# Performance work log

Measured on AMD Instinct MI355X. Metric: run time of the kernel, lower is better.

## Reference

```python
import jax, jax.numpy as jnp
import numpy as np

B, S, E, H = 2, 2048, 1024, 16
D = E // H  # head_dim = 64


def setup_inputs() -> dict:
    key = jax.random.key(0)
    ks = jax.random.split(key, 4)
    return {
        "hidden_states": jax.random.normal(ks[0], (B, S, E), jnp.float32),
        "qk_weight": jax.random.normal(ks[1], (E, 2 * E), jnp.float32) * 0.02,
        "qk_bias": jnp.zeros((2 * E,), jnp.float32),
        "v_weight": jax.random.normal(ks[2], (E, E), jnp.float32) * 0.02,
        "v_resid_gain": jnp.ones((), jnp.float32),
        "v_skip_gain": jnp.ones((), jnp.float32),
        "proj_weight": jax.random.normal(ks[3], (E, E), jnp.float32) * 0.02,
        "proj_resid_gain": jnp.ones((), jnp.float32),
        "proj_skip_gain": jnp.ones((), jnp.float32),
        "attn_mat_resid_gain": jnp.ones((H,), jnp.float32),
        "attn_mat_skip_gain": jnp.ones((H,), jnp.float32),
        "centre_attn_gain": jnp.ones((H,), jnp.float32),
    }


def reference(hidden_states, qk_weight, qk_bias, v_weight, v_resid_gain,
              v_skip_gain, proj_weight, proj_resid_gain, proj_skip_gain,
              attn_mat_resid_gain, attn_mat_skip_gain, centre_attn_gain):
    b, s, e = hidden_states.shape
    dt = hidden_states.dtype
    eye_e = jnp.eye(e, dtype=dt)

    # qk_attn: MyConv1D (standard linear), split into query/key
    qk = hidden_states @ qk_weight + qk_bias
    q, k = jnp.split(qk, 2, axis=-1)
    # v_attn: skip MyConv1D -> x @ (resid_gain * W + skip_gain * I), no bias
    v = hidden_states @ (v_resid_gain * v_weight + v_skip_gain * eye_e)

    def split_heads(t):  # [b,s,e] -> [b,h,s,d]
        return t.reshape(b, s, H, D).transpose(0, 2, 1, 3)

    q, k, v = split_heads(q), split_heads(k), split_heads(v)

    # scaled causal attention scores
    scores = jnp.einsum('bhqd,bhkd->bhqk', q, k) / jnp.asarray(D, dt) ** 0.5
    causal = jnp.tril(jnp.ones((s, s), bool))
    scores = jnp.where(causal, scores, jnp.finfo(dt).min)
    attn = jax.nn.softmax(scores, axis=-1)

    # shaped attention: gain-mix softmax probs with identity and causal-uniform
    uniform = jnp.tril(jnp.ones((s, s), dt) / jnp.arange(1, s + 1, dtype=dt)[:, None])
    g_r = attn_mat_resid_gain[None, :, None, None]
    g_s = attn_mat_skip_gain[None, :, None, None]
    g_c = centre_attn_gain[None, :, None, None]
    new_attn = g_r * attn + g_s * jnp.eye(s, dtype=dt) - g_c * uniform

    ctx = jnp.einsum('bhqk,bhkd->bhqd', new_attn, v)
    ctx = ctx.transpose(0, 2, 1, 3).reshape(b, s, e)  # merge heads
    # c_proj: skip MyConv1D, no bias
    out = ctx @ (proj_resid_gain * proj_weight + proj_skip_gain * eye_e)
    return out
```

## Files before the change

kernel.cpp:

```cpp
#include <hip/hip_runtime.h>

typedef __bf16 bf16;
typedef __attribute__((ext_vector_type(8))) __bf16 bf16x8;
typedef __attribute__((ext_vector_type(4))) float f32x4;

union U16x8 { uint4 u; bf16 h[8]; };
union Pack4 { uint2 u2; bf16 h[4]; };

#define QSCALE 0.18033688011112042f

__device__ __forceinline__ void async16(const bf16* g, bf16* l) {
    __builtin_amdgcn_global_load_lds((const __attribute__((address_space(1))) void*)g,
                                     (__attribute__((address_space(3))) void*)l, 16, 0, 0);
}

__device__ const int QT_OF[40] = {15,15,15,15,14,14,14,14,13,13,13,13,12,12,12,12,
                                  11,11,11,10,10,10,9,9,9,8,8,8,7,7,6,6,5,5,4,4,3,2,1,0};
__device__ const int CK_OF[40] = {0,1,2,3,0,1,2,3,0,1,2,3,0,1,2,3,
                                  0,1,2,0,1,2,0,1,2,0,1,2,0,1,0,1,0,1,0,1,0,0,0,0};
__device__ const int BASE_OF[16] = {39,38,37,36,34,32,30,28,25,22,19,16,12,8,4,0};

__global__ void prep(const float* __restrict__ hs, bf16* __restrict__ hsb,
                     const float* __restrict__ qkw, const float* __restrict__ vw,
                     const float* __restrict__ pw, bf16* __restrict__ qkvT,
                     bf16* __restrict__ pwT, float* __restrict__ csum,
                     const float* __restrict__ vrg, const float* __restrict__ vsg,
                     const float* __restrict__ prg, const float* __restrict__ psg) {
    const int K = 1024;
    int bx = blockIdx.x;
    if (bx < 8) {
        float4* p = (float4*)csum + (bx * 256 + threadIdx.x) * 16;
        #pragma unroll
        for (int i = 0; i < 16; i++) p[i] = make_float4(0.f, 0.f, 0.f, 0.f);
        return;
    }
    if (bx < 4104) {
        int i = ((bx - 8) * 256 + threadIdx.x) * 4;
        float4 f = *(const float4*)(hs + i);
        hsb[i + 0] = (bf16)f.x; hsb[i + 1] = (bf16)f.y;
        hsb[i + 2] = (bf16)f.z; hsb[i + 3] = (bf16)f.w;
        return;
    }
    int r = bx - 4104;
    int z = r < 2048 ? 0 : (r < 3072 ? 1 : 2);
    int q = z == 0 ? r : (z == 1 ? r - 2048 : r - 3072);
    int ntiles = z == 0 ? 64 : 32;
    int N = z == 0 ? 2048 : 1024;
    const float* W = z == 0 ? qkw : (z == 1 ? vw : pw);
    bf16* WT = z == 0 ? qkvT : (z == 1 ? qkvT + (size_t)2 * 1024 * 1024 : pwT);
    float g0 = z == 0 ? 1.f : (z == 1 ? vrg[0] : prg[0]);
    float g1 = z == 0 ? 0.f : (z == 1 ? vsg[0] : psg[0]);

    __shared__ float tile[32][33];
    int n0 = (q % ntiles) * 32, k0 = (q / ntiles) * 32;
    int tx = threadIdx.x & 31, ty = threadIdx.x >> 5;
    #pragma unroll
    for (int rr = 0; rr < 32; rr += 8)
        tile[ty + rr][tx] = W[(size_t)(k0 + ty + rr) * N + n0 + tx];
    __syncthreads();
    #pragma unroll
    for (int rr = 0; rr < 32; rr += 8) {
        int n = n0 + ty + rr, k = k0 + tx;
        float v = g0 * tile[tx][ty + rr] + ((n == k) ? g1 : 0.f);
        if (z == 0 && n < 1024) v *= QSCALE;
        WT[(size_t)n * K + k] = (bf16)v;
    }
}

template<int BN>
__global__ __launch_bounds__(256, 3)
void gemm_bt(const bf16* __restrict__ A, const bf16* __restrict__ BT,
             int M, int N, int K, void* __restrict__ Cout,
             bf16* __restrict__ C2T, float* __restrict__ csum,
             int mode, const float* __restrict__ aux) {
    __shared__ __align__(16) bf16 As[128][64];
    __shared__ __align__(16) bf16 Bs[BN][64];
    constexpr int JF = BN / 32;
    int bid = blockIdx.x;
    int g32 = bid & 31;
    int m0 = ((g32 & 7) * 4 + (g32 >> 3)) * 128;
    int n0 = (bid >> 5) * BN;
    int t = threadIdx.x, lane = t & 63, w = t >> 6;
    int wm = (w >> 1) * 64, wn = (w & 1) * (BN / 2);
    int lrow = lane & 15, lkg = lane >> 4;

    f32x4 acc[4][JF] = {};

    int gsw = ((lane & 7) ^ ((lane >> 3) & 7)) * 8;
    const bf16* Ab = A + (size_t)(m0 + w * 8 + (lane >> 3)) * K + gsw;
    const bf16* Bb = BT + (size_t)(n0 + w * 8 + (lane >> 3)) * K + gsw;

    for (int k0 = 0; k0 < K; k0 += 64) {
        #pragma unroll
        for (int p = 0; p < 4; p++)
            async16(Ab + (size_t)(p * 32) * K + k0, &As[p * 32 + w * 8][0]);
        #pragma unroll
        for (int p = 0; p < BN / 32; p++)
            async16(Bb + (size_t)(p * 32) * K + k0, &Bs[p * 32 + w * 8][0]);
        __syncthreads();
        #pragma unroll
        for (int ks = 0; ks < 2; ks++) {
            bf16x8 af[4], bfr[JF];
            int phys = (((4 * ks + lkg) ^ (lrow & 7)) << 3);
            #pragma unroll
            for (int i = 0; i < 4; i++) af[i] = *(const bf16x8*)&As[wm + i * 16 + lrow][phys];
            #pragma unroll
            for (int j = 0; j < JF; j++) bfr[j] = *(const bf16x8*)&Bs[wn + j * 16 + lrow][phys];
            #pragma unroll
            for (int i = 0; i < 4; i++)
                #pragma unroll
                for (int j = 0; j < JF; j++)
                    acc[i][j] = __builtin_amdgcn_mfma_f32_16x16x32_bf16(af[i], bfr[j], acc[i][j], 0, 0, 0);
        }
        __syncthreads();
    }

    int rgrp = (lane >> 4) * 4;
    #pragma unroll
    for (int i = 0; i < 4; i++) {
        #pragma unroll
        for (int j = 0; j < JF; j++) {
            int col = n0 + wn + j * 16 + lrow;
            int row0 = m0 + wm + i * 16 + rgrp;
            if (mode == 0) {
                if (col < 2048) {
                    float bb = aux[col];
                    if (col < 1024) bb *= QSCALE;
                    #pragma unroll
                    for (int reg = 0; reg < 4; reg++)
                        ((bf16*)Cout)[(size_t)(row0 + reg) * 2048 + col] = (bf16)(acc[i][j][reg] + bb);
                } else {
                    int c = col - 2048;
                    Pack4 p4;
                    #pragma unroll
                    for (int reg = 0; reg < 4; reg++) p4.h[reg] = (bf16)acc[i][j][reg];
                    *(uint2*)&C2T[(size_t)c * 4096 + row0] = p4.u2;
                }
            } else {
                #pragma unroll
                for (int reg = 0; reg < 4; reg++)
                    ((float*)Cout)[(size_t)(row0 + reg) * N + col] = acc[i][j][reg];
            }
        }
    }

    if (mode == 0 && n0 >= 2048) {
        int chunkb = (m0 + wm) >> 5;
        #pragma unroll
        for (int j = 0; j < JF; j++) {
            float s0 = 0.f, s1 = 0.f;
            #pragma unroll
            for (int reg = 0; reg < 4; reg++) {
                s0 += acc[0][j][reg] + acc[1][j][reg];
                s1 += acc[2][j][reg] + acc[3][j][reg];
            }
            s0 += __shfl_xor(s0, 16, 64); s0 += __shfl_xor(s0, 32, 64);
            s1 += __shfl_xor(s1, 16, 64); s1 += __shfl_xor(s1, 32, 64);
            if (lkg == 0) {
                int col = n0 - 2048 + wn + j * 16 + lrow;
                atomicAdd(&csum[(size_t)col * 128 + chunkb], s0);
                atomicAdd(&csum[(size_t)col * 128 + chunkb + 1], s1);
            }
        }
    }
}

__global__ __launch_bounds__(256, 3)
void flash_split(const bf16* __restrict__ qk, const bf16* __restrict__ vT,
                 bf16* __restrict__ Opart, float* __restrict__ lbuf,
                 int S, int E, int H) {
    __shared__ __align__(16) bf16 Ks[2][64][64];
    __shared__ __align__(16) bf16 Vt[2][64][64];
    __shared__ __align__(16) bf16 Ps[4][32][72];

    int item = blockIdx.x, bh = blockIdx.y;
    int qt = QT_OF[item], ck = CK_OF[item];
    int b = bh >> 4, h = bh & 15;
    int q0 = qt * 128;
    int ktstart = ck * 8;
    int nloc = min(8, 2 * (qt + 1) - ktstart);
    int t = threadIdx.x, lane = t & 63, w = t >> 6;
    int lrow = lane & 15, lkg = lane >> 4;
    const int ld = 2 * E;

    const bf16* Qg  = qk + (size_t)(b * S + q0) * ld + h * 64;
    const bf16* Kg0 = qk + (size_t)(b * S) * ld + E + h * 64;
    const bf16* Vg0 = vT + (size_t)(h * 64) * 4096 + b * 2048;

    bf16x8 qf[2][2];
    #pragma unroll
    for (int qg = 0; qg < 2; qg++)
        #pragma unroll
        for (int ks = 0; ks < 2; ks++)
            qf[qg][ks] = *(const bf16x8*)&Qg[(size_t)(32 * w + 16 * qg + lrow) * ld + ks * 32 + lkg * 8];

    f32x4 oacc[4][2] = {};
    float lrun[2] = {0.f, 0.f};

    auto stage = [&](int buf, int kt) {
        int k0 = kt * 64;
        int g = (lane & 7) ^ ((lane >> 3) & 7);
        #pragma unroll
        for (int p = 0; p < 2; p++) {
            int row = w * 8 + p * 32 + (lane >> 3);
            async16(Kg0 + (size_t)(k0 + row) * ld + g * 8, &Ks[buf][row][(lane & 7) * 8]);
            async16(Vg0 + (size_t)row * 4096 + k0 + g * 8, &Vt[buf][row][(lane & 7) * 8]);
        }
    };

    stage(0, ktstart);
    for (int kl = 0; kl < nloc; kl++) {
        int buf = kl & 1;
        int k0 = (ktstart + kl) * 64;
        __syncthreads();
        if (kl + 1 < nloc) stage(1 - buf, ktstart + kl + 1);

        bool skip0 = (k0 > q0 + 32 * w + 15);
        bool skip1 = (k0 > q0 + 32 * w + 31);
        if (skip0 && skip1) continue;

        f32x4 sacc[2][4] = {};
        #pragma unroll
        for (int ks = 0; ks < 2; ks++) {
            bf16x8 ak[4];
            int phys = (((4 * ks + lkg) ^ (lrow & 7)) << 3);
            #pragma unroll
            for (int kf = 0; kf < 4; kf++)
                ak[kf] = *(const bf16x8*)&Ks[buf][16 * kf + lrow][phys];
            #pragma unroll
            for (int kf = 0; kf < 4; kf++)
                sacc[0][kf] = __builtin_amdgcn_mfma_f32_16x16x32_bf16(ak[kf], qf[0][ks], sacc[0][kf], 0, 0, 0);
            if (!skip1)
                #pragma unroll
                for (int kf = 0; kf < 4; kf++)
                    sacc[1][kf] = __builtin_amdgcn_mfma_f32_16x16x32_bf16(ak[kf], qf[1][ks], sacc[1][kf], 0, 0, 0);
        }

        #pragma unroll
        for (int qg = 0; qg < 2; qg++) {
            if ((qg == 0 && skip0) || (qg == 1 && skip1)) continue;
            int kmin = q0 + 32 * w + 16 * qg;
            float rsum = 0.f;
            if (k0 + 63 <= kmin) {
                #pragma unroll
                for (int kf = 0; kf < 4; kf++) {
                    Pack4 p4;
                    #pragma unroll
                    for (int r = 0; r < 4; r++) {
                        float p = exp2f(sacc[qg][kf][r]);
                        rsum += p;
                        p4.h[r] = (bf16)p;
                    }
                    *(uint2*)&Ps[w][16 * qg + lrow][16 * kf + 4 * lkg] = p4.u2;
                }
            } else {
                int qrow = kmin + lrow;
                #pragma unroll
                for (int kf = 0; kf < 4; kf++) {
                    Pack4 p4;
                    #pragma unroll
                    for (int r = 0; r < 4; r++) {
                        float sv = sacc[qg][kf][r];
                        if (k0 + 16 * kf + 4 * lkg + r > qrow) sv = -1e30f;
                        float p = exp2f(sv);
                        rsum += p;
                        p4.h[r] = (bf16)p;
                    }
                    *(uint2*)&Ps[w][16 * qg + lrow][16 * kf + 4 * lkg] = p4.u2;
                }
            }
            lrun[qg] += rsum;
        }

        #pragma unroll
        for (int ks = 0; ks < 2; ks++) {
            bf16x8 av[4];
            int phys = (((4 * ks + lkg) ^ (lrow & 7)) << 3);
            #pragma unroll
            for (int df = 0; df < 4; df++)
                av[df] = *(const bf16x8*)&Vt[buf][16 * df + lrow][phys];
            #pragma unroll
            for (int qg = 0; qg < 2; qg++) {
                if ((qg == 0 && skip0) || (qg == 1 && skip1)) continue;
                bf16x8 bp = *(const bf16x8*)&Ps[w][16 * qg + lrow][ks * 32 + lkg * 8];
                #pragma unroll
                for (int df = 0; df < 4; df++)
                    oacc[df][qg] = __builtin_amdgcn_mfma_f32_16x16x32_bf16(av[df], bp, oacc[df][qg], 0, 0, 0);
            }
        }
    }

    size_t ibase = (size_t)(bh * 40 + item) * 128;
    #pragma unroll
    for (int qg = 0; qg < 2; qg++) {
        #pragma unroll
        for (int df = 0; df < 4; df++) {
            Pack4 p4;
            #pragma unroll
            for (int r = 0; r < 4; r++) p4.h[r] = (bf16)oacc[df][qg][r];
            *(uint2*)&Ps[w][16 * qg + lrow][16 * df + 4 * lkg] = p4.u2;
        }
        float l = lrun[qg];
        l += __shfl_xor(l, 16, 64);
        l += __shfl_xor(l, 32, 64);
        if (lkg == 0) lbuf[ibase + w * 32 + qg * 16 + lrow] = l;
    }
    int r_l = lane >> 1, half = lane & 1;
    bf16* orow = Opart + (ibase + w * 32 + r_l) * 64 + 32 * half;
    #pragma unroll
    for (int c = 0; c < 4; c++)
        *(uint4*)&orow[8 * c] = *(const uint4*)&Ps[w][r_l][32 * half + 8 * c];
}

__global__ void merge_combine(const bf16* __restrict__ Opart, const float* __restrict__ lbuf,
                              const bf16* __restrict__ vT, const float* __restrict__ csum,
                              const float* __restrict__ gr, const float* __restrict__ gs,
                              const float* __restrict__ gc, bf16* __restrict__ ctx) {
    const int S = 2048, E = 1024;
    int qt = blockIdx.x, bh = blockIdx.y;
    int b = bh >> 4, h = bh & 15;
    int nc = (qt >> 2) + 1, base = BASE_OF[qt];
    int q0 = qt * 128;
    int t = threadIdx.x;

    __shared__ bf16 osm[128][66];

    {
        int r = t >> 1, dh = (t & 1) * 32;
        float L = 0.f;
        for (int c = 0; c < nc; c++)
            L += lbuf[(size_t)(bh * 40 + base + c) * 128 + r];
        float inv = 1.f / L;
        float o[32] = {};
        for (int c = 0; c < nc; c++) {
            const bf16* src = Opart + ((size_t)(bh * 40 + base + c) * 128 + r) * 64 + dh;
            #pragma unroll
            for (int g = 0; g < 4; g++) {
                U16x8 u; u.u = *(const uint4*)&src[g * 8];
                #pragma unroll
                for (int j = 0; j < 8; j++) o[g * 8 + j] += (float)u.h[j];
            }
        }
        #pragma unroll
        for (int j = 0; j < 32; j++) osm[r][dh + j] = (bf16)(o[j] * inv);
    }
    __syncthreads();

    {
        int c = t & 63, sc = t >> 6;
        int col = h * 64 + c;
        int row0 = q0 + sc * 32;
        float grh = gr[h], gsh = gs[h], gch = gc[h];
        int cend = qt * 4 + sc;
        const float4* cs4 = (const float4*)(csum + (size_t)col * 128 + b * 64);
        float run = 0.f;
        #pragma unroll
        for (int g = 0; g < 16; g++) {
            float4 f = cs4[g];
            int j = g * 4;
            run += (j + 0 < cend ? f.x : 0.f) + (j + 1 < cend ? f.y : 0.f)
                 + (j + 2 < cend ? f.z : 0.f) + (j + 3 < cend ? f.w : 0.f);
        }
        const bf16* vrow = vT + (size_t)col * 4096 + b * 2048 + row0;
        U16x8 vv[4];
        #pragma unroll
        for (int g = 0; g < 4; g++) vv[g].u = *(const uint4*)&vrow[g * 8];
        bf16* cp = ctx + ((size_t)(b * S + row0)) * E + col;
        #pragma unroll
        for (int i = 0; i < 32; i++) {
            float v = (float)vv[i >> 3].h[i & 7];
            run += v;
            float pm = run / (float)(row0 + i + 1);
            cp[(size_t)i * E] = (bf16)(grh * (float)osm[sc * 32 + i][c] + gsh * v - gch * pm);
        }
    }
}

extern "C" void kernel_launch(void* const* d_in, const int* in_sizes, int n_in,
                              void* d_out, int out_size, void* d_ws, size_t ws_size,
                              hipStream_t stream) {
    const float* hs  = (const float*)d_in[0];
    const float* qkw = (const float*)d_in[1];
    const float* qkb = (const float*)d_in[2];
    const float* vw  = (const float*)d_in[3];
    const float* vrg = (const float*)d_in[4];
    const float* vsg = (const float*)d_in[5];
    const float* pw  = (const float*)d_in[6];
    const float* prg = (const float*)d_in[7];
    const float* psg = (const float*)d_in[8];
    const float* amr = (const float*)d_in[9];
    const float* ams = (const float*)d_in[10];
    const float* amc = (const float*)d_in[11];
    float* out = (float*)d_out;

    const int B = 2, S = 2048, E = 1024, H = 16, M = B * S;
    char* ws = (char*)d_ws;
    size_t off = 0;
    auto alloc = [&](size_t bytes) { void* p = ws + off; off += (bytes + 255) & ~255ull; return p; };
    bf16* hsb   = (bf16*)alloc((size_t)M * E * 2);
    bf16* qkvT  = (bf16*)alloc((size_t)3 * E * E * 2);
    bf16* pwT   = (bf16*)alloc((size_t)E * E * 2);
    bf16* qko   = (bf16*)alloc((size_t)M * 2 * E * 2);
    bf16* vT    = (bf16*)alloc((size_t)E * M * 2);
    float* csum = (float*)alloc((size_t)E * 128 * 4);
    bf16* ctxb  = (bf16*)alloc((size_t)M * E * 2);
    bf16* Opart = (bf16*)alloc((size_t)32 * 40 * 128 * 64 * 2);
    float* lbuf = (float*)alloc((size_t)32 * 40 * 128 * 4);

    prep<<<8200, 256, 0, stream>>>(hs, hsb, qkw, vw, pw, qkvT, pwT, csum, vrg, vsg, prg, psg);

    gemm_bt<128><<<32 * (3 * E / 128), 256, 0, stream>>>(
        hsb, qkvT, M, 3 * E, E, qko, vT, csum, 0, qkb);

    flash_split<<<dim3(40, 32), 256, 0, stream>>>(qko, vT, Opart, lbuf, S, E, H);
    merge_combine<<<dim3(16, 32), 256, 0, stream>>>(Opart, lbuf, vT, csum, amr, ams, amc, ctxb);

    gemm_bt<64><<<32 * (E / 64), 256, 0, stream>>>(
        ctxb, pwT, M, E, E, out, nullptr, nullptr, 2, nullptr);
}
```

Before: 206.9 us.

## Move P tile from LDS into registers via cross-lane shuffles in flash kernel

The softmax probabilities are now packed into registers and redistributed into the MFMA B-operand layout with cross-lane shuffles, instead of going through a per-wave shared-memory P buffer. The K/V buffers are merged into one 32KB array, which is reused as output staging after a barrier. Launch bounds rise from 3 to 5 blocks per SIMD. This cuts LDS footprint and LDS traffic to allow more resident blocks, but adds eight shuffles per MFMA group and may raise register pressure.

```diff
diff --git a/kernel.cpp b/kernel.cpp
--- a/kernel.cpp
+++ b/kernel.cpp
@@ -6,6 +6,8 @@
 
 union U16x8 { uint4 u; bf16 h[8]; };
 union Pack4 { uint2 u2; bf16 h[4]; };
+union PK2 { unsigned u; bf16 h[2]; };
+union BP8 { uint4 u; bf16x8 v; };
 
 #define QSCALE 0.18033688011112042f
 
@@ -165,13 +167,11 @@
     }
 }
 
-__global__ __launch_bounds__(256, 3)
+__global__ __launch_bounds__(256, 5)
 void flash_split(const bf16* __restrict__ qk, const bf16* __restrict__ vT,
                  bf16* __restrict__ Opart, float* __restrict__ lbuf,
                  int S, int E, int H) {
-    __shared__ __align__(16) bf16 Ks[2][64][64];
-    __shared__ __align__(16) bf16 Vt[2][64][64];
-    __shared__ __align__(16) bf16 Ps[4][32][72];
+    __shared__ __align__(16) bf16 smem[16384];
 
     int item = blockIdx.x, bh = blockIdx.y;
     int qt = QT_OF[item], ck = CK_OF[item];
@@ -203,8 +203,8 @@
         #pragma unroll
         for (int p = 0; p < 2; p++) {
             int row = w * 8 + p * 32 + (lane >> 3);
-            async16(Kg0 + (size_t)(k0 + row) * ld + g * 8, &Ks[buf][row][(lane & 7) * 8]);
-            async16(Vg0 + (size_t)row * 4096 + k0 + g * 8, &Vt[buf][row][(lane & 7) * 8]);
+            async16(Kg0 + (size_t)(k0 + row) * ld + g * 8, &smem[buf * 4096 + row * 64 + (lane & 7) * 8]);
+            async16(Vg0 + (size_t)row * 4096 + k0 + g * 8, &smem[8192 + buf * 4096 + row * 64 + (lane & 7) * 8]);
         }
     };
 
@@ -226,7 +226,7 @@
             int phys = (((4 * ks + lkg) ^ (lrow & 7)) << 3);
             #pragma unroll
             for (int kf = 0; kf < 4; kf++)
-                ak[kf] = *(const bf16x8*)&Ks[buf][16 * kf + lrow][phys];
+                ak[kf] = *(const bf16x8*)&smem[buf * 4096 + (16 * kf + lrow) * 64 + phys];
             #pragma unroll
             for (int kf = 0; kf < 4; kf++)
                 sacc[0][kf] = __builtin_amdgcn_mfma_f32_16x16x32_bf16(ak[kf], qf[0][ks], sacc[0][kf], 0, 0, 0);
@@ -236,6 +236,7 @@
                     sacc[1][kf] = __builtin_amdgcn_mfma_f32_16x16x32_bf16(ak[kf], qf[1][ks], sacc[1][kf], 0, 0, 0);
         }
 
+        unsigned plo[2][4], phi[2][4];
         #pragma unroll
         for (int qg = 0; qg < 2; qg++) {
             if ((qg == 0 && skip0) || (qg == 1 && skip1)) continue;
@@ -244,52 +245,66 @@
             if (k0 + 63 <= kmin) {
                 #pragma unroll
                 for (int kf = 0; kf < 4; kf++) {
-                    Pack4 p4;
-                    #pragma unroll
-                    for (int r = 0; r < 4; r++) {
-                        float p = exp2f(sacc[qg][kf][r]);
-                        rsum += p;
-                        p4.h[r] = (bf16)p;
-                    }
-                    *(uint2*)&Ps[w][16 * qg + lrow][16 * kf + 4 * lkg] = p4.u2;
+                    float p0 = exp2f(sacc[qg][kf][0]), p1 = exp2f(sacc[qg][kf][1]);
+                    float p2 = exp2f(sacc[qg][kf][2]), p3 = exp2f(sacc[qg][kf][3]);
+                    rsum += (p0 + p1) + (p2 + p3);
+                    PK2 a; a.h[0] = (bf16)p0; a.h[1] = (bf16)p1; plo[qg][kf] = a.u;
+                    PK2 c; c.h[0] = (bf16)p2; c.h[1] = (bf16)p3; phi[qg][kf] = c.u;
                 }
             } else {
                 int qrow = kmin + lrow;
                 #pragma unroll
                 for (int kf = 0; kf < 4; kf++) {
-                    Pack4 p4;
+                    float pv[4];
                     #pragma unroll
                     for (int r = 0; r < 4; r++) {
                         float sv = sacc[qg][kf][r];
                         if (k0 + 16 * kf + 4 * lkg + r > qrow) sv = -1e30f;
-                        float p = exp2f(sv);
-                        rsum += p;
-                        p4.h[r] = (bf16)p;
+                        pv[r] = exp2f(sv);
+                        rsum += pv[r];
                     }
-                    *(uint2*)&Ps[w][16 * qg + lrow][16 * kf + 4 * lkg] = p4.u2;
+                    PK2 a; a.h[0] = (bf16)pv[0]; a.h[1] = (bf16)pv[1]; plo[qg][kf] = a.u;
+                    PK2 c; c.h[0] = (bf16)pv[2]; c.h[1] = (bf16)pv[3]; phi[qg][kf] = c.u;
                 }
             }
             lrun[qg] += rsum;
         }
 
+        int srcA = 32 * (lkg & 1) + lrow;
+        int srcB = srcA + 16;
+        bool sel = (lkg & 2) != 0;
         #pragma unroll
         for (int ks = 0; ks < 2; ks++) {
             bf16x8 av[4];
             int phys = (((4 * ks + lkg) ^ (lrow & 7)) << 3);
             #pragma unroll
             for (int df = 0; df < 4; df++)
-                av[df] = *(const bf16x8*)&Vt[buf][16 * df + lrow][phys];
+                av[df] = *(const bf16x8*)&smem[8192 + buf * 4096 + (16 * df + lrow) * 64 + phys];
             #pragma unroll
             for (int qg = 0; qg < 2; qg++) {
                 if ((qg == 0 && skip0) || (qg == 1 && skip1)) continue;
-                bf16x8 bp = *(const bf16x8*)&Ps[w][16 * qg + lrow][ks * 32 + lkg * 8];
+                unsigned aL0 = __shfl((int)plo[qg][2 * ks], srcA, 64);
+                unsigned aH0 = __shfl((int)phi[qg][2 * ks], srcA, 64);
+                unsigned aL1 = __shfl((int)plo[qg][2 * ks + 1], srcA, 64);
+                unsigned aH1 = __shfl((int)phi[qg][2 * ks + 1], srcA, 64);
+                unsigned bL0 = __shfl((int)plo[qg][2 * ks], srcB, 64);
+                unsigned bH0 = __shfl((int)phi[qg][2 * ks], srcB, 64);
+                unsigned bL1 = __shfl((int)plo[qg][2 * ks + 1], srcB, 64);
+                unsigned bH1 = __shfl((int)phi[qg][2 * ks + 1], srcB, 64);
+                BP8 W;
+                W.u.x = sel ? aL1 : aL0;
+                W.u.y = sel ? aH1 : aH0;
+                W.u.z = sel ? bL1 : bL0;
+                W.u.w = sel ? bH1 : bH0;
                 #pragma unroll
                 for (int df = 0; df < 4; df++)
-                    oacc[df][qg] = __builtin_amdgcn_mfma_f32_16x16x32_bf16(av[df], bp, oacc[df][qg], 0, 0, 0);
-            }
-        }
-    }
-
+                    oacc[df][qg] = __builtin_amdgcn_mfma_f32_16x16x32_bf16(av[df], W.v, oacc[df][qg], 0, 0, 0);
+            }
+        }
+    }
+
+    __syncthreads();
+    bf16* Sc = smem + w * 32 * 72;
     size_t ibase = (size_t)(bh * 40 + item) * 128;
     #pragma unroll
     for (int qg = 0; qg < 2; qg++) {
@@ -298,7 +313,7 @@
             Pack4 p4;
             #pragma unroll
             for (int r = 0; r < 4; r++) p4.h[r] = (bf16)oacc[df][qg][r];
-            *(uint2*)&Ps[w][16 * qg + lrow][16 * df + 4 * lkg] = p4.u2;
+            *(uint2*)&Sc[(16 * qg + lrow) * 72 + 16 * df + 4 * lkg] = p4.u2;
         }
         float l = lrun[qg];
         l += __shfl_xor(l, 16, 64);
@@ -309,7 +324,7 @@
     bf16* orow = Opart + (ibase + w * 32 + r_l) * 64 + 32 * half;
     #pragma unroll
     for (int c = 0; c < 4; c++)
-        *(uint4*)&orow[8 * c] = *(const uint4*)&Ps[w][r_l][32 * half + 8 * c];
+        *(uint4*)&orow[8 * c] = *(const uint4*)&Sc[r_l * 72 + 32 * half + 8 * c];
 }
 
 __global__ void merge_combine(const bf16* __restrict__ Opart, const float* __restrict__ lbuf,
```

Result: slower. 350.1 us (+69.2%).
